# Optimization experiments

Measured on AMD Instinct MI355X. Metric: run time of the kernel, lower is better.

The kernel has to match this reference:

```python
import jax, jax.numpy as jnp
import numpy as np

DIM = 128
CODEBOOK_SIZE = 1024


def setup_inputs() -> dict:
    key = jax.random.key(0)
    kx, ke = jax.random.split(key)
    x = jax.random.normal(kx, (64, 1500, DIM), dtype=jnp.float32)
    # uniform_init uses kaiming_uniform_ on [K, D]: U(-b, b), b = sqrt(6 / fan_in) with a=sqrt(5) -> gain adjusts bound
    bound = float(np.sqrt(1.0 / DIM))  # kaiming_uniform with a=sqrt(5): bound = sqrt(6/((1+5)*fan_in)) = sqrt(1/fan_in)
    embed = jax.random.uniform(ke, (CODEBOOK_SIZE, DIM), dtype=jnp.float32, minval=-bound, maxval=bound)
    return {"x": x, "embed": embed}


def reference(x, embed):
    # x: [B, T, D], embed: [K, D]
    B, T, D = x.shape
    flat = x.reshape(-1, D)  # [N, D]
    dist = (2.0 * (flat @ embed.T)
            - jnp.sum(flat * flat, axis=-1, keepdims=True)
            - jnp.sum(embed * embed, axis=-1))  # [N, K]
    embed_ind = jnp.argmax(dist, axis=-1).reshape(B, T)  # [B, T]
    quantize = embed[embed_ind]  # [B, T, D] gather
    return quantize, embed_ind
```

## Files before the change

### kernel.cpp

```cpp
#include <hip/hip_runtime.h>
#include <hip/hip_fp16.h>

#define DIM 128
#define KCODES 1024
#define BROWS 128
#define CCHUNK 64
#define NCHUNKS (KCODES / CCHUNK)
#define CH_HALFS (CCHUNK * DIM)
#define TAU_ACC 1.2e-3f

typedef _Float16 f16x8 __attribute__((ext_vector_type(8)));
typedef float f32x4 __attribute__((ext_vector_type(4)));

__device__ __forceinline__ void gl_lds16(const void* g, void* l) {
    __builtin_amdgcn_global_load_lds(
        (const __attribute__((address_space(1))) void*)g,
        (__attribute__((address_space(3))) void*)l, 16, 0, 0);
}

__global__ void enorm_kernel(const float* __restrict__ embed, float* __restrict__ enorm) {
    int k = blockIdx.x * blockDim.x + threadIdx.x;
    if (k < KCODES) {
        const float4* row = (const float4*)(embed + (size_t)k * DIM);
        float s = 0.f;
#pragma unroll
        for (int d = 0; d < DIM / 4; ++d) {
            float4 v = row[d];
            s = fmaf(v.x, v.x, s); s = fmaf(v.y, v.y, s);
            s = fmaf(v.z, v.z, s); s = fmaf(v.w, v.w, s);
        }
        enorm[k] = s;
    }
}

__global__ void pack_kernel(const float* __restrict__ embed, _Float16* __restrict__ Ehp) {
    int t = blockIdx.x * blockDim.x + threadIdx.x;
    int n  = t & 15;
    int q  = (t >> 4) & 3;
    int ks = (t >> 6) & 3;
    int c  = t >> 8;
    const float* src = embed + (size_t)(c * 16 + n) * DIM + ks * 32 + q * 8;
    float4 a0 = *(const float4*)src;
    float4 a1 = *(const float4*)(src + 4);
    float f[8] = {a0.x, a0.y, a0.z, a0.w, a1.x, a1.y, a1.z, a1.w};
    f16x8 h8;
#pragma unroll
    for (int j = 0; j < 8; ++j) h8[j] = (_Float16)f[j];
    *(f16x8*)&Ehp[(size_t)t * 8] = h8;
}

__global__ __launch_bounds__(256, 3)
void argmax_mfma_kernel(const float* __restrict__ x, const float* __restrict__ embed,
                        const _Float16* __restrict__ Ehp, const float* __restrict__ enorm,
                        float* __restrict__ outq, float* __restrict__ outi) {
    __shared__ __align__(16) _Float16 ebuf[2][CH_HALFS];
    __shared__ float enorm_l[KCODES];
    __shared__ int idx_l[BROWS];
    __shared__ int flist[BROWS];
    __shared__ float rbest[4];
    __shared__ int   rbidx[4];
    __shared__ int fcnt;

    const int tid  = threadIdx.x;
    const int w    = tid >> 6;
    const int lane = tid & 63;
    const int n    = lane & 15;
    const int q    = lane >> 4;
    const size_t row0 = (size_t)blockIdx.x * BROWS;

    if (tid == 0) fcnt = 0;
    {
        float4 e4 = ((const float4*)enorm)[tid];
        float4 v; v.x = -0.5f * e4.x; v.y = -0.5f * e4.y; v.z = -0.5f * e4.z; v.w = -0.5f * e4.w;
        ((float4*)enorm_l)[tid] = v;
    }

    {
        const _Float16* gsrc = Ehp + (size_t)w * 2048 + (size_t)lane * 8;
        _Float16* ldst = &ebuf[0][w * 2048];
#pragma unroll
        for (int ks = 0; ks < 4; ++ks)
            gl_lds16(gsrc + ks * 512, ldst + ks * 512);
    }

    f16x8 xh[2][4], xl[2][4];
#pragma unroll
    for (int s = 0; s < 2; ++s)
#pragma unroll
        for (int ks = 0; ks < 4; ++ks) {
            const float* xp = x + (row0 + (size_t)(w * 32 + s * 16 + n)) * DIM + ks * 32 + q * 8;
            float4 a0 = *(const float4*)xp;
            float4 a1 = *(const float4*)(xp + 4);
            float f[8] = {a0.x, a0.y, a0.z, a0.w, a1.x, a1.y, a1.z, a1.w};
            f16x8 h, l;
#pragma unroll
            for (int j = 0; j < 8; ++j) {
                _Float16 hh = (_Float16)f[j];
                h[j] = hh;
                l[j] = (_Float16)(f[j] - (float)hh);
            }
            xh[s][ks] = h; xl[s][ks] = l;
        }

    __syncthreads();

    float best[2][4], sec[2][4]; int bidx[2][4];
#pragma unroll
    for (int s = 0; s < 2; ++s)
#pragma unroll
        for (int rg = 0; rg < 4; ++rg) { best[s][rg] = -3.4e38f; sec[s][rg] = -3.4e38f; bidx[s][rg] = 0; }

#define PROC(CI, EBC, EV) do {                                                        \
    const int code_ = (CI) * 16 + n;                                                  \
    const _Float16* ebc_ = (EBC) + (size_t)lane * 8;                                  \
    f16x8 B0 = *(const f16x8*)(ebc_);                                                 \
    f16x8 B1 = *(const f16x8*)(ebc_ + 512);                                           \
    f16x8 B2 = *(const f16x8*)(ebc_ + 1024);                                          \
    f16x8 B3 = *(const f16x8*)(ebc_ + 1536);                                          \
    f32x4 h0 = {EV, EV, EV, EV}, l0 = {0.f, 0.f, 0.f, 0.f};                           \
    f32x4 h1 = {EV, EV, EV, EV}, l1 = {0.f, 0.f, 0.f, 0.f};                           \
    h0 = __builtin_amdgcn_mfma_f32_16x16x32_f16(xh[0][0], B0, h0, 0, 0, 0);           \
    h1 = __builtin_amdgcn_mfma_f32_16x16x32_f16(xh[1][0], B0, h1, 0, 0, 0);           \
    l0 = __builtin_amdgcn_mfma_f32_16x16x32_f16(xl[0][0], B0, l0, 0, 0, 0);           \
    l1 = __builtin_amdgcn_mfma_f32_16x16x32_f16(xl[1][0], B0, l1, 0, 0, 0);           \
    h0 = __builtin_amdgcn_mfma_f32_16x16x32_f16(xh[0][1], B1, h0, 0, 0, 0);           \
    h1 = __builtin_amdgcn_mfma_f32_16x16x32_f16(xh[1][1], B1, h1, 0, 0, 0);           \
    l0 = __builtin_amdgcn_mfma_f32_16x16x32_f16(xl[0][1], B1, l0, 0, 0, 0);           \
    l1 = __builtin_amdgcn_mfma_f32_16x16x32_f16(xl[1][1], B1, l1, 0, 0, 0);           \
    h0 = __builtin_amdgcn_mfma_f32_16x16x32_f16(xh[0][2], B2, h0, 0, 0, 0);           \
    h1 = __builtin_amdgcn_mfma_f32_16x16x32_f16(xh[1][2], B2, h1, 0, 0, 0);           \
    l0 = __builtin_amdgcn_mfma_f32_16x16x32_f16(xl[0][2], B2, l0, 0, 0, 0);           \
    l1 = __builtin_amdgcn_mfma_f32_16x16x32_f16(xl[1][2], B2, l1, 0, 0, 0);           \
    h0 = __builtin_amdgcn_mfma_f32_16x16x32_f16(xh[0][3], B3, h0, 0, 0, 0);           \
    h1 = __builtin_amdgcn_mfma_f32_16x16x32_f16(xh[1][3], B3, h1, 0, 0, 0);           \
    l0 = __builtin_amdgcn_mfma_f32_16x16x32_f16(xl[0][3], B3, l0, 0, 0, 0);           \
    l1 = __builtin_amdgcn_mfma_f32_16x16x32_f16(xl[1][3], B3, l1, 0, 0, 0);           \
    _Pragma("unroll")                                                                 \
    for (int rg = 0; rg < 4; ++rg) {                                                  \
        float sc0 = h0[rg] + l0[rg];                                                  \
        sec[0][rg]  = __builtin_amdgcn_fmed3f(best[0][rg], sec[0][rg], sc0);          \
        bidx[0][rg] = (sc0 > best[0][rg]) ? code_ : bidx[0][rg];                      \
        best[0][rg] = fmaxf(best[0][rg], sc0);                                        \
        float sc1 = h1[rg] + l1[rg];                                                  \
        sec[1][rg]  = __builtin_amdgcn_fmed3f(best[1][rg], sec[1][rg], sc1);          \
        bidx[1][rg] = (sc1 > best[1][rg]) ? code_ : bidx[1][rg];                      \
        best[1][rg] = fmaxf(best[1][rg], sc1);                                        \
    }                                                                                 \
} while (0)

    int curb = 0;
#pragma unroll 1
    for (int kt = 0; kt < NCHUNKS; ++kt) {
        if (kt + 1 < NCHUNKS) {
            const _Float16* gsrc = Ehp + (size_t)(kt + 1) * CH_HALFS
                                       + (size_t)w * 2048 + (size_t)lane * 8;
            _Float16* ldst = &ebuf[curb ^ 1][w * 2048];
#pragma unroll
            for (int ks = 0; ks < 4; ++ks)
                gl_lds16(gsrc + ks * 512, ldst + ks * 512);
        }
        const _Float16* eb = &ebuf[curb][0];
        float e0 = enorm_l[kt * 64 + n];
        float e1 = enorm_l[kt * 64 + 16 + n];
        float e2 = enorm_l[kt * 64 + 32 + n];
        float e3 = enorm_l[kt * 64 + 48 + n];
        PROC(kt * 4 + 0, eb, e0);
        PROC(kt * 4 + 1, eb + 2048, e1);
        PROC(kt * 4 + 2, eb + 4096, e2);
        PROC(kt * 4 + 3, eb + 6144, e3);
        __syncthreads();
        curb ^= 1;
    }
#undef PROC

#pragma unroll
    for (int mask = 1; mask < 16; mask <<= 1) {
#pragma unroll
        for (int s = 0; s < 2; ++s)
#pragma unroll
            for (int rg = 0; rg < 4; ++rg) {
                float ob = __shfl_xor(best[s][rg], mask);
                float os = __shfl_xor(sec[s][rg], mask);
                int   oi = __shfl_xor(bidx[s][rg], mask);
                if (ob > best[s][rg] || (ob == best[s][rg] && oi < bidx[s][rg])) {
                    sec[s][rg] = fmaxf(best[s][rg], os);
                    best[s][rg] = ob; bidx[s][rg] = oi;
                } else {
                    sec[s][rg] = fmaxf(sec[s][rg], ob);
                }
            }
    }
    if (n == 0) {
#pragma unroll
        for (int s = 0; s < 2; ++s)
#pragma unroll
            for (int rg = 0; rg < 4; ++rg) {
                int r = w * 32 + s * 16 + q * 4 + rg;
                idx_l[r] = bidx[s][rg];
                if (best[s][rg] - sec[s][rg] < TAU_ACC) {
                    int p = atomicAdd(&fcnt, 1);
                    flist[p] = r;
                }
            }
    }
    __syncthreads();

    int nf = fcnt;
    for (int f = 0; f < nf; ++f) {
        int r = flist[f];
        const float4* xg4 = (const float4*)(x + (row0 + r) * DIM);
        float b = -3.4e38f; int bi = 0;
        int cbase = w * 256 + lane * 4;
        for (int c = cbase; c < cbase + 4; ++c) {
            const float4* eg4 = (const float4*)(embed + (size_t)c * DIM);
            float s = 0.f;
#pragma unroll 8
            for (int d = 0; d < DIM / 4; ++d) {
                float4 xv = xg4[d], ev = eg4[d];
                s = fmaf(xv.x, ev.x, s); s = fmaf(xv.y, ev.y, s);
                s = fmaf(xv.z, ev.z, s); s = fmaf(xv.w, ev.w, s);
            }
            float sc = fmaf(2.f, s, -enorm[c]);
            if (sc > b) { b = sc; bi = c; }
        }
#pragma unroll
        for (int mask = 1; mask < 64; mask <<= 1) {
            float ob = __shfl_xor(b, mask);
            int   oi = __shfl_xor(bi, mask);
            if (ob > b || (ob == b && oi < bi)) { b = ob; bi = oi; }
        }
        if (lane == 0) { rbest[w] = b; rbidx[w] = bi; }
        __syncthreads();
        if (tid == 0) {
            float B = rbest[0]; int BI = rbidx[0];
#pragma unroll
            for (int i = 1; i < 4; ++i)
                if (rbest[i] > B || (rbest[i] == B && rbidx[i] < BI)) { B = rbest[i]; BI = rbidx[i]; }
            idx_l[r] = BI;
        }
        __syncthreads();
    }
    __syncthreads();

    const float4* e4 = (const float4*)embed;
    float4* oq4 = (float4*)outq + row0 * (DIM / 4);
#pragma unroll
    for (int i = 0; i < 16; ++i) {
        int g = tid + i * 256;
        int r = g >> 5, d4 = g & 31;
        int id = idx_l[r];
        oq4[g] = e4[(size_t)id * (DIM / 4) + d4];
    }
    if (tid < BROWS) outi[row0 + tid] = (float)idx_l[tid];
}

extern "C" void kernel_launch(void* const* d_in, const int* in_sizes, int n_in,
                              void* d_out, int out_size, void* d_ws, size_t ws_size,
                              hipStream_t stream) {
    const float* x     = (const float*)d_in[0];
    const float* embed = (const float*)d_in[1];
    const int x_elems  = in_sizes[0];
    const int n_rows   = x_elems / DIM;

    float*    enorm = (float*)d_ws;
    _Float16* Ehp   = (_Float16*)((char*)d_ws + 4096);

    float* outq = (float*)d_out;
    float* outi = (float*)d_out + (size_t)x_elems;

    enorm_kernel<<<KCODES / 256, 256, 0, stream>>>(embed, enorm);
    pack_kernel<<<KCODES * 16 / 256, 256, 0, stream>>>(embed, Ehp);
    argmax_mfma_kernel<<<n_rows / BROWS, 256, 0, stream>>>(x, embed, Ehp, enorm, outq, outi);
}
```

Measured before the change: 243.8 us.

## Drop split-fp16 low-part MFMAs and deepen codebook pipeline to four buffers

```diff
diff --git a/kernel.cpp b/kernel.cpp
--- a/kernel.cpp
+++ b/kernel.cpp
@@ -4,10 +4,10 @@
 #define DIM 128
 #define KCODES 1024
 #define BROWS 128
-#define CCHUNK 64
-#define NCHUNKS (KCODES / CCHUNK)
-#define CH_HALFS (CCHUNK * DIM)
-#define TAU_ACC 1.2e-3f
+#define CCH 32
+#define NCHK (KCODES / CCH)
+#define NBUF 4
+#define TAU_ACC 3.0e-3f
 
 typedef _Float16 f16x8 __attribute__((ext_vector_type(8)));
 typedef float f32x4 __attribute__((ext_vector_type(4)));
@@ -49,11 +49,11 @@
     *(f16x8*)&Ehp[(size_t)t * 8] = h8;
 }
 
-__global__ __launch_bounds__(256, 3)
+__global__ __launch_bounds__(256, 4)
 void argmax_mfma_kernel(const float* __restrict__ x, const float* __restrict__ embed,
                         const _Float16* __restrict__ Ehp, const float* __restrict__ enorm,
                         float* __restrict__ outq, float* __restrict__ outi) {
-    __shared__ __align__(16) _Float16 ebuf[2][CH_HALFS];
+    __shared__ __align__(16) _Float16 ebuf[NBUF][CCH * DIM];
     __shared__ float enorm_l[KCODES];
     __shared__ int idx_l[BROWS];
     __shared__ int flist[BROWS];
@@ -75,15 +75,15 @@
         ((float4*)enorm_l)[tid] = v;
     }
 
-    {
-        const _Float16* gsrc = Ehp + (size_t)w * 2048 + (size_t)lane * 8;
-        _Float16* ldst = &ebuf[0][w * 2048];
-#pragma unroll
-        for (int ks = 0; ks < 4; ++ks)
-            gl_lds16(gsrc + ks * 512, ldst + ks * 512);
-    }
-
-    f16x8 xh[2][4], xl[2][4];
+#pragma unroll
+    for (int pt = 0; pt < 3; ++pt) {
+        const _Float16* gsrc = Ehp + (size_t)pt * (CCH * DIM) + (size_t)(w * 1024) + (size_t)lane * 8;
+        _Float16* ldst = &ebuf[pt][w * 1024];
+        gl_lds16(gsrc, ldst);
+        gl_lds16(gsrc + 512, ldst + 512);
+    }
+
+    f16x8 xh[2][4];
 #pragma unroll
     for (int s = 0; s < 2; ++s)
 #pragma unroll
@@ -92,14 +92,10 @@
             float4 a0 = *(const float4*)xp;
             float4 a1 = *(const float4*)(xp + 4);
             float f[8] = {a0.x, a0.y, a0.z, a0.w, a1.x, a1.y, a1.z, a1.w};
-            f16x8 h, l;
-#pragma unroll
-            for (int j = 0; j < 8; ++j) {
-                _Float16 hh = (_Float16)f[j];
-                h[j] = hh;
-                l[j] = (_Float16)(f[j] - (float)hh);
-            }
-            xh[s][ks] = h; xl[s][ks] = l;
+            f16x8 h;
+#pragma unroll
+            for (int j = 0; j < 8; ++j) h[j] = (_Float16)f[j];
+            xh[s][ks] = h;
         }
 
     __syncthreads();
@@ -113,63 +109,45 @@
 #define PROC(CI, EBC, EV) do {                                                        \
     const int code_ = (CI) * 16 + n;                                                  \
     const _Float16* ebc_ = (EBC) + (size_t)lane * 8;                                  \
-    f16x8 B0 = *(const f16x8*)(ebc_);                                                 \
-    f16x8 B1 = *(const f16x8*)(ebc_ + 512);                                           \
-    f16x8 B2 = *(const f16x8*)(ebc_ + 1024);                                          \
-    f16x8 B3 = *(const f16x8*)(ebc_ + 1536);                                          \
-    f32x4 h0 = {EV, EV, EV, EV}, l0 = {0.f, 0.f, 0.f, 0.f};                           \
-    f32x4 h1 = {EV, EV, EV, EV}, l1 = {0.f, 0.f, 0.f, 0.f};                           \
-    h0 = __builtin_amdgcn_mfma_f32_16x16x32_f16(xh[0][0], B0, h0, 0, 0, 0);           \
-    h1 = __builtin_amdgcn_mfma_f32_16x16x32_f16(xh[1][0], B0, h1, 0, 0, 0);           \
-    l0 = __builtin_amdgcn_mfma_f32_16x16x32_f16(xl[0][0], B0, l0, 0, 0, 0);           \
-    l1 = __builtin_amdgcn_mfma_f32_16x16x32_f16(xl[1][0], B0, l1, 0, 0, 0);           \
-    h0 = __builtin_amdgcn_mfma_f32_16x16x32_f16(xh[0][1], B1, h0, 0, 0, 0);           \
-    h1 = __builtin_amdgcn_mfma_f32_16x16x32_f16(xh[1][1], B1, h1, 0, 0, 0);           \
-    l0 = __builtin_amdgcn_mfma_f32_16x16x32_f16(xl[0][1], B1, l0, 0, 0, 0);           \
-    l1 = __builtin_amdgcn_mfma_f32_16x16x32_f16(xl[1][1], B1, l1, 0, 0, 0);           \
-    h0 = __builtin_amdgcn_mfma_f32_16x16x32_f16(xh[0][2], B2, h0, 0, 0, 0);           \
-    h1 = __builtin_amdgcn_mfma_f32_16x16x32_f16(xh[1][2], B2, h1, 0, 0, 0);           \
-    l0 = __builtin_amdgcn_mfma_f32_16x16x32_f16(xl[0][2], B2, l0, 0, 0, 0);           \
-    l1 = __builtin_amdgcn_mfma_f32_16x16x32_f16(xl[1][2], B2, l1, 0, 0, 0);           \
-    h0 = __builtin_amdgcn_mfma_f32_16x16x32_f16(xh[0][3], B3, h0, 0, 0, 0);           \
-    h1 = __builtin_amdgcn_mfma_f32_16x16x32_f16(xh[1][3], B3, h1, 0, 0, 0);           \
-    l0 = __builtin_amdgcn_mfma_f32_16x16x32_f16(xl[0][3], B3, l0, 0, 0, 0);           \
-    l1 = __builtin_amdgcn_mfma_f32_16x16x32_f16(xl[1][3], B3, l1, 0, 0, 0);           \
+    f32x4 a0 = {EV, EV, EV, EV};                                                      \
+    f32x4 a1 = {EV, EV, EV, EV};                                                      \
+    _Pragma("unroll")                                                                 \
+    for (int ks_ = 0; ks_ < 4; ++ks_) {                                               \
+        f16x8 B = *(const f16x8*)(ebc_ + ks_ * 512);                                  \
+        a0 = __builtin_amdgcn_mfma_f32_16x16x32_f16(xh[0][ks_], B, a0, 0, 0, 0);      \
+        a1 = __builtin_amdgcn_mfma_f32_16x16x32_f16(xh[1][ks_], B, a1, 0, 0, 0);      \
+    }                                                                                 \
     _Pragma("unroll")                                                                 \
     for (int rg = 0; rg < 4; ++rg) {                                                  \
-        float sc0 = h0[rg] + l0[rg];                                                  \
+        float sc0 = a0[rg];                                                           \
         sec[0][rg]  = __builtin_amdgcn_fmed3f(best[0][rg], sec[0][rg], sc0);          \
         bidx[0][rg] = (sc0 > best[0][rg]) ? code_ : bidx[0][rg];                      \
         best[0][rg] = fmaxf(best[0][rg], sc0);                                        \
-        float sc1 = h1[rg] + l1[rg];                                                  \
+        float sc1 = a1[rg];                                                           \
         sec[1][rg]  = __builtin_amdgcn_fmed3f(best[1][rg], sec[1][rg], sc1);          \
         bidx[1][rg] = (sc1 > best[1][rg]) ? code_ : bidx[1][rg];                      \
         best[1][rg] = fmaxf(best[1][rg], sc1);                                        \
     }                                                                                 \
 } while (0)
 
-    int curb = 0;
 #pragma unroll 1
-    for (int kt = 0; kt < NCHUNKS; ++kt) {
-        if (kt + 1 < NCHUNKS) {
-            const _Float16* gsrc = Ehp + (size_t)(kt + 1) * CH_HALFS
-                                       + (size_t)w * 2048 + (size_t)lane * 8;
-            _Float16* ldst = &ebuf[curb ^ 1][w * 2048];
-#pragma unroll
-            for (int ks = 0; ks < 4; ++ks)
-                gl_lds16(gsrc + ks * 512, ldst + ks * 512);
-        }
-        const _Float16* eb = &ebuf[curb][0];
-        float e0 = enorm_l[kt * 64 + n];
-        float e1 = enorm_l[kt * 64 + 16 + n];
-        float e2 = enorm_l[kt * 64 + 32 + n];
-        float e3 = enorm_l[kt * 64 + 48 + n];
-        PROC(kt * 4 + 0, eb, e0);
-        PROC(kt * 4 + 1, eb + 2048, e1);
-        PROC(kt * 4 + 2, eb + 4096, e2);
-        PROC(kt * 4 + 3, eb + 6144, e3);
-        __syncthreads();
-        curb ^= 1;
+    for (int t = 0; t < NCHK; ++t) {
+        {
+            const int tc = (t + 3) & (NCHK - 1);
+            const _Float16* gsrc = Ehp + (size_t)tc * (CCH * DIM) + (size_t)(w * 1024) + (size_t)lane * 8;
+            _Float16* ldst = &ebuf[(t + 3) & (NBUF - 1)][w * 1024];
+            gl_lds16(gsrc, ldst);
+            gl_lds16(gsrc + 512, ldst + 512);
+        }
+        const _Float16* eb = &ebuf[t & (NBUF - 1)][0];
+        float e0 = enorm_l[t * CCH + n];
+        float e1 = enorm_l[t * CCH + 16 + n];
+        __builtin_amdgcn_s_setprio(1);
+        PROC(t * 2,     eb,        e0);
+        PROC(t * 2 + 1, eb + 2048, e1);
+        __builtin_amdgcn_s_setprio(0);
+        asm volatile("s_waitcnt vmcnt(4)" ::: "memory");
+        __builtin_amdgcn_s_barrier();
     }
 #undef PROC
 
```

New measurement: 301.0 us. 23.5% more time.
